# Kernel tuning notes

Measured on AMD Instinct MI355X. Metric: run time of the kernel, lower is better.

## Reference

```python
import jax, jax.numpy as jnp
import numpy as np

B, S, E = 2, 2048, 1024
H = 16
HD = E // H  # 64


def setup_inputs() -> dict:
    key = jax.random.key(0)
    ks = jax.random.split(key, 9)
    sc = 1.0 / np.sqrt(E)
    return {
        "X": jax.random.normal(ks[0], (B, S, E), jnp.float32),
        "Wq": jax.random.normal(ks[1], (E, E), jnp.float32) * sc,
        "bq": jax.random.normal(ks[2], (E,), jnp.float32) * sc,
        "Wk": jax.random.normal(ks[3], (E, E), jnp.float32) * sc,
        "bk": jax.random.normal(ks[4], (E,), jnp.float32) * sc,
        "Wv": jax.random.normal(ks[5], (E, E), jnp.float32) * sc,
        "bv": jax.random.normal(ks[6], (E,), jnp.float32) * sc,
        "Wo": jax.random.normal(ks[7], (E, E), jnp.float32) * sc,
        "bo": jax.random.normal(ks[8], (E,), jnp.float32) * sc,
    }


def reference(X, Wq, bq, Wk, bk, Wv, bv, Wo, bo):
    b, s, e = X.shape
    # torch Linear: x @ W.T + b (weights stored (out, in))
    Q = X @ Wq.T + bq
    K = X @ Wk.T + bk
    V = X @ Wv.T + bv
    # (b, s, E) -> (b, H, s, HD)
    Q = Q.reshape(b, s, H, HD).transpose(0, 2, 1, 3)
    K = K.reshape(b, s, H, HD).transpose(0, 2, 1, 3)
    V = V.reshape(b, s, H, HD).transpose(0, 2, 1, 3)
    scores = jnp.einsum("bhqd,bhkd->bhqk", Q, K) / np.sqrt(HD).astype(np.float32)
    attn = jax.nn.softmax(scores, axis=-1)
    ctx = jnp.einsum("bhqk,bhkd->bhqd", attn, V)  # (b, H, s, HD)
    # Faithful to original: reshape (b,H,s,HD) -> (b,s,E) WITHOUT permuting heads back
    ctx = ctx.reshape(b, s, e)
    return ctx @ Wo.T + bo
```

## Files before the change

### kernel.cpp

```cpp
#include <hip/hip_runtime.h>


typedef __bf16 bf16x8 __attribute__((ext_vector_type(8)));
typedef __bf16 bf16x4 __attribute__((ext_vector_type(4)));
typedef float f32x4 __attribute__((ext_vector_type(4)));
typedef unsigned short ushort_t;

#define S_LEN 2048
#define E_DIM 1024
#define H_NUM 16
#define HD_DIM 64

__device__ __forceinline__ ushort_t f2bf(float f) {
  union { float f; unsigned u; } v; v.f = f;
  unsigned u = v.u;
  unsigned r = (u + 0x7FFFu + ((u >> 16) & 1u)) >> 16;
  return (ushort_t)r;
}

#define GLDS16(gp, lp)                                              \
  __builtin_amdgcn_global_load_lds(                                 \
      (const __attribute__((address_space(1))) unsigned int*)(gp),  \
      (__attribute__((address_space(3))) unsigned int*)(lp), 16, 0, 0)

__global__ __launch_bounds__(256) void cvt_f32_bf16(
    const float* __restrict__ src, ushort_t* __restrict__ dst, int n4) {
  int i = blockIdx.x * 256 + threadIdx.x;
  if (i < n4) {
    float4 v = ((const float4*)src)[i];
    ushort4 o;
    o.x = f2bf(v.x); o.y = f2bf(v.y); o.z = f2bf(v.z); o.w = f2bf(v.w);
    ((ushort4*)dst)[i] = o;
  }
}

__global__ __launch_bounds__(256) void gemm_qkv(
    const ushort_t* __restrict__ Xbf, const ushort_t* __restrict__ Wqkv,
    const float* __restrict__ bq, const float* __restrict__ bk,
    const float* __restrict__ bv,
    ushort_t* __restrict__ Qb, ushort_t* __restrict__ Kb,
    ushort_t* __restrict__ Vb) {
  __shared__ ushort_t As[128 * 64];
  __shared__ ushort_t Bs[128 * 64];
  const int t = threadIdx.x;
  const int w = t >> 6, lane = t & 63, quad = lane >> 4, lr = lane & 15;
  const int m0 = blockIdx.y * 128, n0 = blockIdx.x * 128;
  const int wm = (w & 1) * 64, wn = (w >> 1) * 64;
  const int matid = n0 >> 10;
  const int nl0 = n0 & 1023;

  const int srow = t >> 3;
  const int gsrc = (t & 7) ^ (srow & 7);
  const ushort_t* Ag = Xbf + (size_t)(m0 + srow) * E_DIM + gsrc * 8;
  const ushort_t* Bg = Wqkv + (size_t)matid * E_DIM * E_DIM +
                       (size_t)(nl0 + srow) * E_DIM + gsrc * 8;

  f32x4 acc[4][4] = {};

  for (int kt = 0; kt < E_DIM / 64; ++kt) {
#pragma unroll
    for (int r = 0; r < 4; r++) {
      GLDS16(Ag + (size_t)r * 32 * E_DIM, As + r * 2048 + t * 8);
      GLDS16(Bg + (size_t)r * 32 * E_DIM, Bs + r * 2048 + t * 8);
    }
    Ag += 64; Bg += 64;
    __syncthreads();
#pragma unroll
    for (int kk = 0; kk < 2; kk++) {
      bf16x8 af[4], bfr[4];
      const int gs0 = (kk * 4 + quad) ^ (lr & 7);
#pragma unroll
      for (int i = 0; i < 4; i++) {
        af[i]  = *(const bf16x8*)(As + (wm + i * 16 + lr) * 64 + gs0 * 8);
        bfr[i] = *(const bf16x8*)(Bs + (wn + i * 16 + lr) * 64 + gs0 * 8);
      }
#pragma unroll
      for (int i = 0; i < 4; i++)
#pragma unroll
        for (int j = 0; j < 4; j++)
          acc[i][j] = __builtin_amdgcn_mfma_f32_16x16x32_bf16(
              af[i], bfr[j], acc[i][j], 0, 0, 0);
    }
    __syncthreads();
  }

  const float* bias_p = (matid == 0) ? bq : (matid == 1) ? bk : bv;
  ushort_t* dst = (matid == 0) ? Qb : (matid == 1) ? Kb : Vb;
  const float scl = (matid == 0) ? 0.125f : 1.0f;
#pragma unroll
  for (int j = 0; j < 4; j++) {
    int col = n0 + wn + j * 16 + lr;
    int cl = col & 1023;
    int h = cl >> 6, d = cl & 63;
    float bias = bias_p[cl];
#pragma unroll
    for (int i = 0; i < 4; i++) {
#pragma unroll
      for (int r = 0; r < 4; r++) {
        int row = m0 + wm + i * 16 + quad * 4 + r;
        int bb = row >> 11, ss = row & 2047;
        size_t o = ((size_t)((bb * H_NUM + h) * S_LEN + ss)) * HD_DIM + d;
        dst[o] = f2bf((acc[i][j][r] + bias) * scl);
      }
    }
  }
}

__global__ __launch_bounds__(256) void vtrans(
    const ushort_t* __restrict__ Vb, ushort_t* __restrict__ Vt) {
  __shared__ ushort_t tile[64 * 72];
  const int bh = blockIdx.y;
  const int s0 = blockIdx.x * 64;
  const int t = threadIdx.x;
  {
    const int sr = t >> 2, c0 = (t & 3) * 16;
    const ushort_t* src = Vb + ((size_t)bh * S_LEN + s0 + sr) * HD_DIM + c0;
    *(uint4*)(&tile[sr * 72 + c0]) = *(const uint4*)(src);
    *(uint4*)(&tile[sr * 72 + c0 + 8]) = *(const uint4*)(src + 8);
  }
  __syncthreads();
  const int d = t >> 2, c = t & 3;
  ushort_t v[16];
#pragma unroll
  for (int w = 0; w < 16; w++) {
    int key = (w & 3) * 16 + 4 * c + (w >> 2);
    v[w] = tile[key * 72 + d];
  }
  ushort_t* dst = Vt + ((size_t)bh * HD_DIM + d) * S_LEN + s0 + 16 * c;
  *(uint4*)(dst) = *(const uint4*)(v);
  *(uint4*)(dst + 8) = *(const uint4*)(v + 8);
}

__global__ __launch_bounds__(256) void attn(
    const ushort_t* __restrict__ Qb, const ushort_t* __restrict__ Kb,
    const ushort_t* __restrict__ Vt, ushort_t* __restrict__ Ctx) {
  __shared__ ushort_t KV[2 * 64 * 64];
  __shared__ ushort_t Ps[128 * 72];
  ushort_t* Ks = KV;
  ushort_t* Vs = KV + 4096;
  const int t = threadIdx.x, w = t >> 6, lane = t & 63;
  const int quad = lane >> 4, lr = lane & 15;
  const int bh = blockIdx.y, q0 = blockIdx.x * 128;
  const ushort_t* Qg = Qb + ((size_t)bh * S_LEN + q0) * HD_DIM;
  const ushort_t* Kg = Kb + (size_t)bh * S_LEN * HD_DIM;
  const ushort_t* Vg = Vt + (size_t)bh * HD_DIM * S_LEN;

  const int srow = t >> 3;
  const int gsrc = (t & 7) ^ (srow & 7);

#pragma unroll
  for (int r = 0; r < 4; r++)
    GLDS16(Qg + (size_t)(r * 32 + srow) * HD_DIM + gsrc * 8,
           KV + r * 2048 + t * 8);
  __syncthreads();
  bf16x8 qf[2][2];
#pragma unroll
  for (int mt = 0; mt < 2; mt++)
#pragma unroll
    for (int kc = 0; kc < 2; kc++) {
      int row = w * 32 + mt * 16 + lr;
      int gs = (kc * 4 + quad) ^ (lr & 7);
      qf[mt][kc] = *(const bf16x8*)(KV + row * 64 + gs * 8);
    }

  f32x4 cacc[2][4] = {};
  float psum[2][4] = {};

  for (int kt = 0; kt < S_LEN / 64; ++kt) {
    const int k0 = kt * 64;
    __syncthreads();
#pragma unroll
    for (int r = 0; r < 2; r++) {
      GLDS16(Kg + (size_t)(k0 + r * 32 + srow) * HD_DIM + gsrc * 8,
             Ks + r * 2048 + t * 8);
      GLDS16(Vg + (size_t)(r * 32 + srow) * S_LEN + k0 + gsrc * 8,
             Vs + r * 2048 + t * 8);
    }
    __syncthreads();

    f32x4 sacc[2][4] = {};
#pragma unroll
    for (int nt = 0; nt < 4; nt++) {
#pragma unroll
      for (int kc = 0; kc < 2; kc++) {
        int gs = (kc * 4 + quad) ^ (lr & 7);
        bf16x8 kf = *(const bf16x8*)(Ks + (nt * 16 + lr) * 64 + gs * 8);
        sacc[0][nt] = __builtin_amdgcn_mfma_f32_16x16x32_bf16(
            qf[0][kc], kf, sacc[0][nt], 0, 0, 0);
        sacc[1][nt] = __builtin_amdgcn_mfma_f32_16x16x32_bf16(
            qf[1][kc], kf, sacc[1][nt], 0, 0, 0);
      }
    }

#pragma unroll
    for (int mt = 0; mt < 2; mt++) {
#pragma unroll
      for (int i = 0; i < 4; i++) {
        float p0 = __expf(sacc[mt][0][i]);
        float p1 = __expf(sacc[mt][1][i]);
        float p2 = __expf(sacc[mt][2][i]);
        float p3 = __expf(sacc[mt][3][i]);
        psum[mt][i] += (p0 + p1) + (p2 + p3);
        bf16x4 pv;
        pv[0] = (__bf16)p0; pv[1] = (__bf16)p1;
        pv[2] = (__bf16)p2; pv[3] = (__bf16)p3;
        int row = w * 32 + mt * 16 + quad * 4 + i;
        *(bf16x4*)(Ps + row * 72 + lr * 4) = pv;
      }
    }

#pragma unroll
    for (int kc = 0; kc < 2; kc++) {
      bf16x8 vf[4];
#pragma unroll
      for (int dt = 0; dt < 4; dt++) {
        int gs = (kc * 4 + quad) ^ (lr & 7);
        vf[dt] = *(const bf16x8*)(Vs + (dt * 16 + lr) * 64 + gs * 8);
      }
#pragma unroll
      for (int mt = 0; mt < 2; mt++) {
        bf16x8 pf = *(const bf16x8*)(Ps + (w * 32 + mt * 16 + lr) * 72 +
                                     kc * 32 + quad * 8);
#pragma unroll
        for (int dt = 0; dt < 4; dt++)
          cacc[mt][dt] = __builtin_amdgcn_mfma_f32_16x16x32_bf16(
              pf, vf[dt], cacc[mt][dt], 0, 0, 0);
      }
    }
  }

#pragma unroll
  for (int mt = 0; mt < 2; mt++) {
#pragma unroll
    for (int i = 0; i < 4; i++) {
      float rs = psum[mt][i];
      rs += __shfl_xor(rs, 1);
      rs += __shfl_xor(rs, 2);
      rs += __shfl_xor(rs, 4);
      rs += __shfl_xor(rs, 8);
      float inv = 1.0f / rs;
      int srow2 = q0 + w * 32 + mt * 16 + quad * 4 + i;
#pragma unroll
      for (int dt = 0; dt < 4; dt++)
        Ctx[((size_t)bh * S_LEN + srow2) * HD_DIM + dt * 16 + lr] =
            f2bf(cacc[mt][dt][i] * inv);
    }
  }
}

__global__ __launch_bounds__(256) void gemm_out(
    const ushort_t* __restrict__ Cb, const ushort_t* __restrict__ Wob,
    const float* __restrict__ bo, float* __restrict__ out) {
  __shared__ ushort_t As[128 * 64];
  __shared__ ushort_t Bs[128 * 64];
  const int t = threadIdx.x;
  const int w = t >> 6, lane = t & 63, quad = lane >> 4, lr = lane & 15;
  const int m0 = blockIdx.y * 128, n0 = blockIdx.x * 128;
  const int wm = (w & 1) * 64, wn = (w >> 1) * 64;

  const int srow = t >> 3;
  const int gsrc = (t & 7) ^ (srow & 7);
  const ushort_t* Ag = Cb + (size_t)(m0 + srow) * E_DIM + gsrc * 8;
  const ushort_t* Bg = Wob + (size_t)(n0 + srow) * E_DIM + gsrc * 8;

  f32x4 acc[4][4] = {};

  for (int kt = 0; kt < E_DIM / 64; ++kt) {
#pragma unroll
    for (int r = 0; r < 4; r++) {
      GLDS16(Ag + (size_t)r * 32 * E_DIM, As + r * 2048 + t * 8);
      GLDS16(Bg + (size_t)r * 32 * E_DIM, Bs + r * 2048 + t * 8);
    }
    Ag += 64; Bg += 64;
    __syncthreads();
#pragma unroll
    for (int kk = 0; kk < 2; kk++) {
      bf16x8 af[4], bfr[4];
      const int gs0 = (kk * 4 + quad) ^ (lr & 7);
#pragma unroll
      for (int i = 0; i < 4; i++) {
        af[i]  = *(const bf16x8*)(As + (wm + i * 16 + lr) * 64 + gs0 * 8);
        bfr[i] = *(const bf16x8*)(Bs + (wn + i * 16 + lr) * 64 + gs0 * 8);
      }
#pragma unroll
      for (int i = 0; i < 4; i++)
#pragma unroll
        for (int j = 0; j < 4; j++)
          acc[i][j] = __builtin_amdgcn_mfma_f32_16x16x32_bf16(
              af[i], bfr[j], acc[i][j], 0, 0, 0);
    }
    __syncthreads();
  }

#pragma unroll
  for (int j = 0; j < 4; j++) {
    int col = n0 + wn + j * 16 + lr;
    float bias = bo[col];
#pragma unroll
    for (int i = 0; i < 4; i++) {
#pragma unroll
      for (int r = 0; r < 4; r++) {
        int row = m0 + wm + i * 16 + quad * 4 + r;
        out[(size_t)row * E_DIM + col] = acc[i][j][r] + bias;
      }
    }
  }
}

extern "C" void kernel_launch(void* const* d_in, const int* in_sizes, int n_in,
                              void* d_out, int out_size, void* d_ws,
                              size_t ws_size, hipStream_t stream) {
  const float* X  = (const float*)d_in[0];
  const float* bq = (const float*)d_in[2];
  const float* bk = (const float*)d_in[4];
  const float* bv = (const float*)d_in[6];
  const float* Wo = (const float*)d_in[7];
  const float* bo = (const float*)d_in[8];
  float* out = (float*)d_out;

  char* ws = (char*)d_ws;
  ushort_t* Xbf  = (ushort_t*)(ws);
  ushort_t* Wqkv = (ushort_t*)(ws + ((size_t)8 << 20));
  ushort_t* Wob  = (ushort_t*)(ws + ((size_t)14 << 20));
  ushort_t* Qb   = (ushort_t*)(ws + ((size_t)16 << 20));
  ushort_t* Kb   = (ushort_t*)(ws + ((size_t)24 << 20));
  ushort_t* Vb   = (ushort_t*)(ws + ((size_t)32 << 20));
  ushort_t* Vt   = (ushort_t*)(ws + ((size_t)40 << 20));
  ushort_t* Cb   = (ushort_t*)(ws + ((size_t)48 << 20));

  cvt_f32_bf16<<<4096, 256, 0, stream>>>(X, Xbf, 1048576);
  cvt_f32_bf16<<<1024, 256, 0, stream>>>((const float*)d_in[1], Wqkv, 262144);
  cvt_f32_bf16<<<1024, 256, 0, stream>>>((const float*)d_in[3],
                                         Wqkv + (1 << 20), 262144);
  cvt_f32_bf16<<<1024, 256, 0, stream>>>((const float*)d_in[5],
                                         Wqkv + (2 << 20), 262144);
  cvt_f32_bf16<<<1024, 256, 0, stream>>>(Wo, Wob, 262144);

  gemm_qkv<<<dim3(24, 32), 256, 0, stream>>>(Xbf, Wqkv, bq, bk, bv, Qb, Kb, Vb);
  vtrans<<<dim3(32, 32), 256, 0, stream>>>(Vb, Vt);
  attn<<<dim3(16, 32), 256, 0, stream>>>(Qb, Kb, Vt, Cb);
  gemm_out<<<dim3(8, 32), 256, 0, stream>>>(Cb, Wob, bo, out);
}
```

Baseline: 215.9 us.

## Merge conversion launches into one kernel and halve attention query tile

The five separate f32-to-bf16 conversion launches become one kernel that selects its source and destination by global index, which removes launch overhead. The attention kernel now handles 64 query rows per block instead of 128 (16 per wave), doubling the grid to 1024 blocks for better CU occupancy and smaller per-block LDS. The trade-off is that each K/V tile is loaded from global memory twice as often and each loaded K/V fragment feeds half as many MFMAs.

```diff
diff --git a/kernel.cpp b/kernel.cpp
--- a/kernel.cpp
+++ b/kernel.cpp
@@ -23,15 +23,30 @@
       (const __attribute__((address_space(1))) unsigned int*)(gp),  \
       (__attribute__((address_space(3))) unsigned int*)(lp), 16, 0, 0)
 
-__global__ __launch_bounds__(256) void cvt_f32_bf16(
-    const float* __restrict__ src, ushort_t* __restrict__ dst, int n4) {
+__global__ __launch_bounds__(256) void cvt_all(
+    const float* __restrict__ X, const float* __restrict__ Wq,
+    const float* __restrict__ Wk, const float* __restrict__ Wv,
+    const float* __restrict__ Wo, ushort_t* __restrict__ Xbf,
+    ushort_t* __restrict__ Wqkv, ushort_t* __restrict__ Wob) {
   int i = blockIdx.x * 256 + threadIdx.x;
-  if (i < n4) {
-    float4 v = ((const float4*)src)[i];
-    ushort4 o;
-    o.x = f2bf(v.x); o.y = f2bf(v.y); o.z = f2bf(v.z); o.w = f2bf(v.w);
-    ((ushort4*)dst)[i] = o;
-  }
+  const float* src;
+  ushort_t* dst;
+  int off;
+  if (i < 1048576) {
+    src = X; dst = Xbf; off = i;
+  } else if (i < 1310720) {
+    src = Wq; dst = Wqkv; off = i - 1048576;
+  } else if (i < 1572864) {
+    src = Wk; dst = Wqkv + (1 << 20); off = i - 1310720;
+  } else if (i < 1835008) {
+    src = Wv; dst = Wqkv + (2 << 20); off = i - 1572864;
+  } else {
+    src = Wo; dst = Wob; off = i - 1835008;
+  }
+  float4 v = ((const float4*)src)[off];
+  ushort4 o;
+  o.x = f2bf(v.x); o.y = f2bf(v.y); o.z = f2bf(v.z); o.w = f2bf(v.w);
+  ((ushort4*)dst)[off] = o;
 }
 
 __global__ __launch_bounds__(256) void gemm_qkv(
@@ -135,12 +150,12 @@
     const ushort_t* __restrict__ Qb, const ushort_t* __restrict__ Kb,
     const ushort_t* __restrict__ Vt, ushort_t* __restrict__ Ctx) {
   __shared__ ushort_t KV[2 * 64 * 64];
-  __shared__ ushort_t Ps[128 * 72];
+  __shared__ ushort_t Ps[64 * 72];
   ushort_t* Ks = KV;
   ushort_t* Vs = KV + 4096;
   const int t = threadIdx.x, w = t >> 6, lane = t & 63;
   const int quad = lane >> 4, lr = lane & 15;
-  const int bh = blockIdx.y, q0 = blockIdx.x * 128;
+  const int bh = blockIdx.y, q0 = blockIdx.x * 64;
   const ushort_t* Qg = Qb + ((size_t)bh * S_LEN + q0) * HD_DIM;
   const ushort_t* Kg = Kb + (size_t)bh * S_LEN * HD_DIM;
   const ushort_t* Vg = Vt + (size_t)bh * HD_DIM * S_LEN;
@@ -149,22 +164,20 @@
   const int gsrc = (t & 7) ^ (srow & 7);
 
 #pragma unroll
-  for (int r = 0; r < 4; r++)
+  for (int r = 0; r < 2; r++)
     GLDS16(Qg + (size_t)(r * 32 + srow) * HD_DIM + gsrc * 8,
            KV + r * 2048 + t * 8);
   __syncthreads();
-  bf16x8 qf[2][2];
-#pragma unroll
-  for (int mt = 0; mt < 2; mt++)
-#pragma unroll
-    for (int kc = 0; kc < 2; kc++) {
-      int row = w * 32 + mt * 16 + lr;
-      int gs = (kc * 4 + quad) ^ (lr & 7);
-      qf[mt][kc] = *(const bf16x8*)(KV + row * 64 + gs * 8);
-    }
-
-  f32x4 cacc[2][4] = {};
-  float psum[2][4] = {};
+  bf16x8 qf[2];
+#pragma unroll
+  for (int kc = 0; kc < 2; kc++) {
+    int row = w * 16 + lr;
+    int gs = (kc * 4 + quad) ^ (lr & 7);
+    qf[kc] = *(const bf16x8*)(KV + row * 64 + gs * 8);
+  }
+
+  f32x4 cacc[4] = {};
+  float psum[4] = {};
 
   for (int kt = 0; kt < S_LEN / 64; ++kt) {
     const int k0 = kt * 64;
@@ -178,73 +191,59 @@
     }
     __syncthreads();
 
-    f32x4 sacc[2][4] = {};
+    f32x4 sacc[4] = {};
 #pragma unroll
     for (int nt = 0; nt < 4; nt++) {
 #pragma unroll
       for (int kc = 0; kc < 2; kc++) {
         int gs = (kc * 4 + quad) ^ (lr & 7);
         bf16x8 kf = *(const bf16x8*)(Ks + (nt * 16 + lr) * 64 + gs * 8);
-        sacc[0][nt] = __builtin_amdgcn_mfma_f32_16x16x32_bf16(
-            qf[0][kc], kf, sacc[0][nt], 0, 0, 0);
-        sacc[1][nt] = __builtin_amdgcn_mfma_f32_16x16x32_bf16(
-            qf[1][kc], kf, sacc[1][nt], 0, 0, 0);
-      }
-    }
-
-#pragma unroll
-    for (int mt = 0; mt < 2; mt++) {
-#pragma unroll
-      for (int i = 0; i < 4; i++) {
-        float p0 = __expf(sacc[mt][0][i]);
-        float p1 = __expf(sacc[mt][1][i]);
-        float p2 = __expf(sacc[mt][2][i]);
-        float p3 = __expf(sacc[mt][3][i]);
-        psum[mt][i] += (p0 + p1) + (p2 + p3);
-        bf16x4 pv;
-        pv[0] = (__bf16)p0; pv[1] = (__bf16)p1;
-        pv[2] = (__bf16)p2; pv[3] = (__bf16)p3;
-        int row = w * 32 + mt * 16 + quad * 4 + i;
-        *(bf16x4*)(Ps + row * 72 + lr * 4) = pv;
-      }
+        sacc[nt] = __builtin_amdgcn_mfma_f32_16x16x32_bf16(
+            qf[kc], kf, sacc[nt], 0, 0, 0);
+      }
+    }
+
+#pragma unroll
+    for (int i = 0; i < 4; i++) {
+      float p0 = __expf(sacc[0][i]);
+      float p1 = __expf(sacc[1][i]);
+      float p2 = __expf(sacc[2][i]);
+      float p3 = __expf(sacc[3][i]);
+      psum[i] += (p0 + p1) + (p2 + p3);
+      bf16x4 pv;
+      pv[0] = (__bf16)p0; pv[1] = (__bf16)p1;
+      pv[2] = (__bf16)p2; pv[3] = (__bf16)p3;
+      int row = w * 16 + quad * 4 + i;
+      *(bf16x4*)(Ps + row * 72 + lr * 4) = pv;
     }
 
 #pragma unroll
     for (int kc = 0; kc < 2; kc++) {
-      bf16x8 vf[4];
+      bf16x8 pf =
+          *(const bf16x8*)(Ps + (w * 16 + lr) * 72 + kc * 32 + quad * 8);
 #pragma unroll
       for (int dt = 0; dt < 4; dt++) {
         int gs = (kc * 4 + quad) ^ (lr & 7);
-        vf[dt] = *(const bf16x8*)(Vs + (dt * 16 + lr) * 64 + gs * 8);
-      }
-#pragma unroll
-      for (int mt = 0; mt < 2; mt++) {
-        bf16x8 pf = *(const bf16x8*)(Ps + (w * 32 + mt * 16 + lr) * 72 +
-                                     kc * 32 + quad * 8);
-#pragma unroll
-        for (int dt = 0; dt < 4; dt++)
-          cacc[mt][dt] = __builtin_amdgcn_mfma_f32_16x16x32_bf16(
-              pf, vf[dt], cacc[mt][dt], 0, 0, 0);
-      }
-    }
-  }
-
-#pragma unroll
-  for (int mt = 0; mt < 2; mt++) {
-#pragma unroll
-    for (int i = 0; i < 4; i++) {
-      float rs = psum[mt][i];
-      rs += __shfl_xor(rs, 1);
-      rs += __shfl_xor(rs, 2);
-      rs += __shfl_xor(rs, 4);
-      rs += __shfl_xor(rs, 8);
-      float inv = 1.0f / rs;
-      int srow2 = q0 + w * 32 + mt * 16 + quad * 4 + i;
-#pragma unroll
-      for (int dt = 0; dt < 4; dt++)
-        Ctx[((size_t)bh * S_LEN + srow2) * HD_DIM + dt * 16 + lr] =
-            f2bf(cacc[mt][dt][i] * inv);
-    }
+        bf16x8 vf = *(const bf16x8*)(Vs + (dt * 16 + lr) * 64 + gs * 8);
+        cacc[dt] = __builtin_amdgcn_mfma_f32_16x16x32_bf16(
+            pf, vf, cacc[dt], 0, 0, 0);
+      }
+    }
+  }
+
+#pragma unroll
+  for (int i = 0; i < 4; i++) {
+    float rs = psum[i];
+    rs += __shfl_xor(rs, 1);
+    rs += __shfl_xor(rs, 2);
+    rs += __shfl_xor(rs, 4);
+    rs += __shfl_xor(rs, 8);
+    float inv = 1.0f / rs;
+    int srow2 = q0 + w * 16 + quad * 4 + i;
+#pragma unroll
+    for (int dt = 0; dt < 4; dt++)
+      Ctx[((size_t)bh * S_LEN + srow2) * HD_DIM + dt * 16 + lr] =
+          f2bf(cacc[dt][i] * inv);
   }
 }
 
@@ -328,16 +327,12 @@
   ushort_t* Vt   = (ushort_t*)(ws + ((size_t)40 << 20));
   ushort_t* Cb   = (ushort_t*)(ws + ((size_t)48 << 20));
 
-  cvt_f32_bf16<<<4096, 256, 0, stream>>>(X, Xbf, 1048576);
-  cvt_f32_bf16<<<1024, 256, 0, stream>>>((const float*)d_in[1], Wqkv, 262144);
-  cvt_f32_bf16<<<1024, 256, 0, stream>>>((const float*)d_in[3],
-                                         Wqkv + (1 << 20), 262144);
-  cvt_f32_bf16<<<1024, 256, 0, stream>>>((const float*)d_in[5],
-                                         Wqkv + (2 << 20), 262144);
-  cvt_f32_bf16<<<1024, 256, 0, stream>>>(Wo, Wob, 262144);
+  cvt_all<<<8192, 256, 0, stream>>>(X, (const float*)d_in[1],
+                                    (const float*)d_in[3],
+                                    (const float*)d_in[5], Wo, Xbf, Wqkv, Wob);
 
   gemm_qkv<<<dim3(24, 32), 256, 0, stream>>>(Xbf, Wqkv, bq, bk, bv, Qb, Kb, Vb);
   vtrans<<<dim3(32, 32), 256, 0, stream>>>(Vb, Vt);
-  attn<<<dim3(16, 32), 256, 0, stream>>>(Qb, Kb, Vt, Cb);
+  attn<<<dim3(32, 32), 256, 0, stream>>>(Qb, Kb, Vt, Cb);
   gemm_out<<<dim3(8, 32), 256, 0, stream>>>(Cb, Wob, bo, out);
 }
```

Result: no change. 212.1 us (-1.8%).
